# Kernel tuning notes

Hardware: AMD Instinct MI355X
Metric: run time of the kernel (lower is better)

## Reference

```python
import jax, jax.numpy as jnp
import numpy as np

EPS = 1e-8  # torch cosine_similarity denominator clamp


def setup_inputs() -> dict:
    key = jax.random.key(0)
    k1, k2, k3 = jax.random.split(key, 3)
    x = jax.random.normal(k1, (4, 512, 256, 256), dtype=jnp.float32)
    v0 = jax.random.normal(k2, (4, 256, 14, 14), dtype=jnp.float32)
    v1 = jax.random.normal(k3, (4, 256, 14, 14), dtype=jnp.float32)
    return {"x": x, "v0": v0, "v1": v1}


def reference(x, v0, v1):
    # CoLoc_Sel.AV_default_forward with C=2, att_type='cos'
    C = 2
    B, D, F, T = x.shape
    Dc = D // C
    H, W = v0.shape[2], v0.shape[3]

    # AdaptiveMaxPool3d((None,1,1)) on (B,D,F,T): global max over (F,T)
    xp = jnp.max(x, axis=(2, 3)).reshape(B, C, Dc)          # (B,C,Dc) = split blocks
    # x_p1 = blocks in order, x_p2 = reversed; stacked -> permutations P=2
    x_t = jnp.stack([xp, xp[:, ::-1]], axis=1)              # (B,P,C,Dc)

    v_cat = jnp.stack([v0, v1], axis=1)                     # (B,C,Dc,H,W)

    # cosine similarity along the Dc axis, broadcast over P and (H,W)
    dot = jnp.einsum('bpcd,bcdhw->bpchw', x_t, v_cat)       # (B,P,C,H,W)
    xn = jnp.sqrt(jnp.sum(x_t * x_t, axis=3))               # (B,P,C)
    vn = jnp.sqrt(jnp.sum(v_cat * v_cat, axis=2))           # (B,C,H,W)
    maps = dot / jnp.maximum(xn[..., None, None] * vn[:, None], EPS)  # (B,P,C,H,W)

    # per-permutation score: max over (H,W), sum over C
    scores = jnp.sum(jnp.max(maps, axis=(3, 4)), axis=-1)   # (B,P)
    order = jnp.argsort(-scores, axis=1)                    # descending
    ss = jnp.take_along_axis(scores, order, axis=1)
    match_loss = jnp.mean(-ss[:, 0] + jnp.sum(ss[:, 1:], axis=-1))

    maps_sorted = jnp.take_along_axis(maps, order[:, :, None, None, None], axis=1)
    att_maps = maps_sorted[:, 0]                            # (B,C,H,W)

    # pick visual feature vector at argmax spatial location of each att map
    max_ind = jnp.argmax(att_maps.reshape(B, C, H * W), axis=-1)        # (B,C)
    v_flat = v_cat.reshape(B, C, Dc, H * W)
    v_sel = jnp.take_along_axis(v_flat, max_ind[:, :, None, None], axis=3)  # (B,C,Dc,1)

    feats = [jnp.broadcast_to(v_sel[:, c, :, :, None], (B, Dc, F, T)) for c in range(C)]
    out = jnp.concatenate([*feats, x], axis=1)              # (B, 2*D, F, T)
    return out, match_loss, att_maps
```

## Files before the change

### kernel.cpp

```cpp
#include <hip/hip_runtime.h>
#include <hip/hip_bf16.h>
#include <float.h>
#include <math.h>

constexpr int B  = 4;
constexpr int D  = 512;
constexpr int C  = 2;
constexpr int Dc = 256;
constexpr int F  = 256;
constexpr int T  = 256;
constexpr int FT = F * T;
constexpr int H  = 14;
constexpr int W  = 14;
constexpr int HW = H * W;
constexpr int OUTC = 2 * Dc + D;
constexpr float EPSV = 1e-8f;

typedef float f4 __attribute__((ext_vector_type(4)));


__global__ __launch_bounds__(256) void kA_maxcopy(const float* __restrict__ x,
                                                  float* __restrict__ out,
                                                  float* __restrict__ xp) {
    const int slice = blockIdx.x;
    const int b = slice / D;
    const int d = slice % D;
    const f4* xs = (const f4*)(x + (size_t)slice * FT);
    f4* os = (f4*)(out + ((size_t)(b * OUTC + 2 * Dc + d)) * FT);
    float m = -FLT_MAX;
    for (int i0 = threadIdx.x; i0 < FT / 4; i0 += 256 * 8) {
        f4 v[8];
        #pragma unroll
        for (int u = 0; u < 8; ++u)
            v[u] = __builtin_nontemporal_load(&xs[i0 + u * 256]);
        #pragma unroll
        for (int u = 0; u < 8; ++u) {
            __builtin_nontemporal_store(v[u], &os[i0 + u * 256]);
            m = fmaxf(m, fmaxf(fmaxf(v[u].x, v[u].y), fmaxf(v[u].z, v[u].w)));
        }
    }
    for (int off = 32; off; off >>= 1) m = fmaxf(m, __shfl_down(m, off, 64));
    __shared__ float sm[4];
    const int lane = threadIdx.x & 63, wid = threadIdx.x >> 6;
    if (lane == 0) sm[wid] = m;
    __syncthreads();
    if (threadIdx.x == 0) {
        float r = sm[0];
        for (int w2 = 1; w2 < 4; ++w2) r = fmaxf(r, sm[w2]);
        xp[slice] = r;
    }
}

__global__ __launch_bounds__(256) void kB_maps(const float* __restrict__ v0,
                                               const float* __restrict__ v1,
                                               const float* __restrict__ xp,
                                               float* __restrict__ maps,
                                               float* __restrict__ mx,
                                               int* __restrict__ amax) {
    const int bc = blockIdx.x;
    const int b = bc / C, c = bc % C;
    const int tid = threadIdx.x;

    __shared__ float sxc[Dc], sxo[Dc];
    sxc[tid] = xp[(b * C + c) * Dc + tid];
    sxo[tid] = xp[(b * C + (1 - c)) * Dc + tid];
    __syncthreads();

    float ec = sxc[tid] * sxc[tid];
    float eo = sxo[tid] * sxo[tid];
    for (int off = 32; off; off >>= 1) {
        ec += __shfl_down(ec, off, 64);
        eo += __shfl_down(eo, off, 64);
    }
    __shared__ float red[8];
    const int lane = tid & 63, wid = tid >> 6;
    if (lane == 0) { red[wid] = ec; red[4 + wid] = eo; }
    __syncthreads();
    __shared__ float s_xn_c, s_xn_o;
    if (tid == 0) {
        s_xn_c = sqrtf(red[0] + red[1] + red[2] + red[3]);
        s_xn_o = sqrtf(red[4] + red[5] + red[6] + red[7]);
    }
    __syncthreads();
    const float xn_c = s_xn_c, xn_o = s_xn_o;

    float map0 = -FLT_MAX, map1 = -FLT_MAX;
    if (tid < HW) {
        const float* vv = (c == 0 ? v0 : v1) + (size_t)b * Dc * HW;
        float d0 = 0.f, d1 = 0.f, vs = 0.f;
        for (int dc = 0; dc < Dc; ++dc) {
            float v = vv[dc * HW + tid];
            d0 = fmaf(sxc[dc], v, d0);
            d1 = fmaf(sxo[dc], v, d1);
            vs = fmaf(v, v, vs);
        }
        float vn = sqrtf(vs);
        map0 = d0 / fmaxf(xn_c * vn, EPSV);
        map1 = d1 / fmaxf(xn_o * vn, EPSV);
        maps[((b * 2 + 0) * C + c) * HW + tid] = map0;
        maps[((b * 2 + 1) * C + c) * HW + tid] = map1;
    }

    __shared__ float rv[256];
    __shared__ int ri[256];
    for (int p = 0; p < 2; ++p) {
        __syncthreads();
        rv[tid] = (tid < HW) ? (p == 0 ? map0 : map1) : -FLT_MAX;
        ri[tid] = tid;
        __syncthreads();
        for (int s = 128; s; s >>= 1) {
            if (tid < s) {
                float v2 = rv[tid + s]; int i2 = ri[tid + s];
                if (v2 > rv[tid] || (v2 == rv[tid] && i2 < ri[tid])) {
                    rv[tid] = v2; ri[tid] = i2;
                }
            }
            __syncthreads();
        }
        if (tid == 0) {
            mx[(b * 2 + p) * C + c] = rv[0];
            amax[(b * 2 + p) * C + c] = ri[0];
        }
    }
}

__global__ __launch_bounds__(256) void kC_select(const float* __restrict__ maps,
                                                 const float* __restrict__ mx,
                                                 const int* __restrict__ amax,
                                                 float* __restrict__ out,
                                                 int* __restrict__ mind) {
    __shared__ int pbest[B];
    const int tid = threadIdx.x;
    if (tid == 0) {
        float L = 0.f;
        for (int b = 0; b < B; ++b) {
            float s0 = mx[(b * 2 + 0) * C + 0] + mx[(b * 2 + 0) * C + 1];
            float s1 = mx[(b * 2 + 1) * C + 0] + mx[(b * 2 + 1) * C + 1];
            int p = (s1 > s0) ? 1 : 0;
            pbest[b] = p;
            float ss0 = p ? s1 : s0;
            float ss1 = p ? s0 : s1;
            L += (ss1 - ss0);
        }
        out[(size_t)B * OUTC * FT] = L / (float)B;
    }
    __syncthreads();
    const size_t att_off = (size_t)B * OUTC * FT + 1;
    for (int i = tid; i < B * C * HW; i += blockDim.x) {
        int b = i / (C * HW);
        int r = i % (C * HW);
        int c = r / HW;
        int hw = r % HW;
        out[att_off + i] = maps[((b * 2 + pbest[b]) * C + c) * HW + hw];
    }
    if (tid < B * C) {
        int b = tid / C, c = tid % C;
        mind[tid] = amax[(b * 2 + pbest[b]) * C + c];
    }
}

__global__ __launch_bounds__(256) void kD_fill(const float* __restrict__ v0,
                                               const float* __restrict__ v1,
                                               const int* __restrict__ mind,
                                               float* __restrict__ out) {
    const int n = blockIdx.x;
    const int b = n / (2 * Dc);
    const int r = n % (2 * Dc);
    const int c = r / Dc;
    const int dc = r % Dc;
    const int hw = mind[b * C + c];
    const float* vv = (c == 0 ? v0 : v1);
    const float val = vv[((size_t)(b * Dc + dc)) * HW + hw];
    f4 v4 = {val, val, val, val};
    f4* os = (f4*)(out + ((size_t)(b * OUTC + c * Dc + dc)) * FT);
    for (int i0 = threadIdx.x; i0 < FT / 4; i0 += 256 * 8) {
        #pragma unroll
        for (int u = 0; u < 8; ++u)
            __builtin_nontemporal_store(v4, &os[i0 + u * 256]);
    }
}

extern "C" void kernel_launch(void* const* d_in, const int* in_sizes, int n_in,
                              void* d_out, int out_size, void* d_ws, size_t ws_size,
                              hipStream_t stream) {
    const float* x  = (const float*)d_in[0];
    const float* v0 = (const float*)d_in[1];
    const float* v1 = (const float*)d_in[2];
    float* out = (float*)d_out;
    float* ws = (float*)d_ws;

    float* xp   = ws;
    float* maps = ws + 2048;
    float* mx   = ws + 5184;
    int*   amax = (int*)(ws + 5200);
    int*   mind = (int*)(ws + 5216);

    kA_maxcopy<<<B * D, 256, 0, stream>>>(x, out, xp);
    kB_maps<<<B * C, 256, 0, stream>>>(v0, v1, xp, maps, mx, amax);
    kC_select<<<1, 256, 0, stream>>>(maps, mx, amax, out, mind);
    kD_fill<<<B * 2 * Dc, 256, 0, stream>>>(v0, v1, mind, out);
}
```

Baseline: 304.0 us.

## Fuse all stages into one cooperative persistent kernel with grid syncs

```diff
diff --git a/kernel.cpp b/kernel.cpp
--- a/kernel.cpp
+++ b/kernel.cpp
@@ -1,23 +1,180 @@
 #include <hip/hip_runtime.h>
 #include <hip/hip_bf16.h>
+#include <hip/hip_cooperative_groups.h>
 #include <float.h>
 #include <math.h>
+
+namespace cg = cooperative_groups;
 
 constexpr int B  = 4;
 constexpr int D  = 512;
 constexpr int C  = 2;
 constexpr int Dc = 256;
-constexpr int F  = 256;
-constexpr int T  = 256;
-constexpr int FT = F * T;
-constexpr int H  = 14;
-constexpr int W  = 14;
-constexpr int HW = H * W;
+constexpr int FT = 256 * 256;
+constexpr int HW = 14 * 14;
 constexpr int OUTC = 2 * Dc + D;
 constexpr float EPSV = 1e-8f;
 
 typedef float f4 __attribute__((ext_vector_type(4)));
 
+__global__ __launch_bounds__(256, 4) void k_fused(const float* __restrict__ x,
+                                                  const float* __restrict__ v0,
+                                                  const float* __restrict__ v1,
+                                                  float* __restrict__ out,
+                                                  float* __restrict__ ws) {
+    cg::grid_group grid = cg::this_grid();
+    const int tid = threadIdx.x;
+    const int blk = blockIdx.x;
+
+    float* xp   = ws;
+    float* pd0  = ws + 2048;
+    float* pd1  = ws + 10240;
+    float* pvs  = ws + 18432;
+    float* maps = ws + 26624;
+    int*   mind = (int*)(ws + 29760);
+
+    __shared__ float sm[4];
+    __shared__ float s_xn[8];
+    __shared__ float s_mx[16];
+    __shared__ int   s_ai[16];
+    __shared__ int   s_pb[B];
+    __shared__ float cand_v[256];
+    __shared__ int   cand_i[256];
+
+    for (int s = 0; s < 2; ++s) {
+        const int slice = blk * 2 + s;
+        const int b = slice / D, d = slice % D;
+        const f4* xs = (const f4*)(x + (size_t)slice * FT);
+        f4* os = (f4*)(out + ((size_t)(b * OUTC + 2 * Dc + d)) * FT);
+        float m = -FLT_MAX;
+        for (int i0 = tid; i0 < FT / 4; i0 += 256 * 8) {
+            f4 v[8];
+            #pragma unroll
+            for (int u = 0; u < 8; ++u)
+                v[u] = __builtin_nontemporal_load(&xs[i0 + u * 256]);
+            #pragma unroll
+            for (int u = 0; u < 8; ++u) {
+                __builtin_nontemporal_store(v[u], &os[i0 + u * 256]);
+                m = fmaxf(m, fmaxf(fmaxf(v[u].x, v[u].y), fmaxf(v[u].z, v[u].w)));
+            }
+        }
+        for (int off = 32; off; off >>= 1) m = fmaxf(m, __shfl_down(m, off, 64));
+        if ((tid & 63) == 0) sm[tid >> 6] = m;
+        __syncthreads();
+        if (tid == 0) xp[slice] = fmaxf(fmaxf(sm[0], sm[1]), fmaxf(sm[2], sm[3]));
+        __syncthreads();
+    }
+    grid.sync();
+
+    if (blk < 32) {
+        const int b = blk >> 3, c = (blk >> 2) & 1, q = blk & 3;
+        if (tid < HW) {
+            const float* vv = (c == 0 ? v0 : v1) + (size_t)b * Dc * HW;
+            const float* xc = xp + (b * C + c) * Dc;
+            const float* xo = xp + (b * C + (1 - c)) * Dc;
+            float d0 = 0.f, d1 = 0.f, vs = 0.f;
+            for (int dc = q * 64; dc < q * 64 + 64; ++dc) {
+                float v = vv[dc * HW + tid];
+                d0 = fmaf(xc[dc], v, d0);
+                d1 = fmaf(xo[dc], v, d1);
+                vs = fmaf(v, v, vs);
+            }
+            pd0[blk * 256 + tid] = d0;
+            pd1[blk * 256 + tid] = d1;
+            pvs[blk * 256 + tid] = vs;
+        }
+    }
+    grid.sync();
+
+    if (blk == 0) {
+        {
+            const int g = tid >> 5, l = tid & 31;
+            float acc = 0.f;
+            for (int dc = l; dc < Dc; dc += 32) {
+                float v = xp[g * Dc + dc];
+                acc = fmaf(v, v, acc);
+            }
+            for (int off = 16; off; off >>= 1) acc += __shfl_down(acc, off, 32);
+            if (l == 0) s_xn[g] = sqrtf(acc);
+        }
+        __syncthreads();
+        for (int i = tid; i < 16 * HW; i += 256) {
+            const int row = i / HW;
+            const int hw = i % HW;
+            const int b = row >> 2, p = (row >> 1) & 1, c = row & 1;
+            const int base = b * 8 + c * 4;
+            float d = 0.f, vs = 0.f;
+            for (int q = 0; q < 4; ++q) {
+                const int o = (base + q) * 256 + hw;
+                d += (p == 0 ? pd0[o] : pd1[o]);
+                vs += pvs[o];
+            }
+            const float xn = (p == 0) ? s_xn[b * C + c] : s_xn[b * C + (1 - c)];
+            maps[i] = d / fmaxf(xn * sqrtf(vs), EPSV);
+        }
+        __syncthreads();
+        {
+            const int row = tid >> 4, sub = tid & 15;
+            float bv = -FLT_MAX; int bi = HW;
+            for (int hw = sub; hw < HW; hw += 16) {
+                float v = maps[row * HW + hw];
+                if (v > bv) { bv = v; bi = hw; }
+            }
+            cand_v[tid] = bv; cand_i[tid] = bi;
+            __syncthreads();
+            if (sub == 0) {
+                float mv = -FLT_MAX; int mi = 0;
+                for (int k = 0; k < 16; ++k) {
+                    float v = cand_v[row * 16 + k]; int idx = cand_i[row * 16 + k];
+                    if (v > mv || (v == mv && idx < mi)) { mv = v; mi = idx; }
+                }
+                s_mx[row] = mv; s_ai[row] = mi;
+            }
+        }
+        __syncthreads();
+        if (tid == 0) {
+            float L = 0.f;
+            for (int b = 0; b < B; ++b) {
+                const float s0 = s_mx[b * 4 + 0] + s_mx[b * 4 + 1];
+                const float s1 = s_mx[b * 4 + 2] + s_mx[b * 4 + 3];
+                const int p = (s1 > s0) ? 1 : 0;
+                s_pb[b] = p;
+                L += p ? (s0 - s1) : (s1 - s0);
+            }
+            out[(size_t)B * OUTC * FT] = L / (float)B;
+        }
+        __syncthreads();
+        const size_t att_off = (size_t)B * OUTC * FT + 1;
+        for (int i = tid; i < B * C * HW; i += 256) {
+            const int b = i / (C * HW);
+            const int r = i % (C * HW);
+            const int c = r / HW, hw = r % HW;
+            out[att_off + i] = maps[(b * 4 + s_pb[b] * 2 + c) * HW + hw];
+        }
+        if (tid < B * C) {
+            const int b = tid / C, c = tid % C;
+            mind[tid] = s_ai[b * 4 + s_pb[b] * 2 + c];
+        }
+    }
+    grid.sync();
+
+    for (int s = 0; s < 2; ++s) {
+        const int slice = blk * 2 + s;
+        const int b = slice / (2 * Dc);
+        const int r = slice % (2 * Dc);
+        const int c = r / Dc, dc = r % Dc;
+        const int hw = mind[b * C + c];
+        const float* vv = (c == 0 ? v0 : v1);
+        const float val = vv[((size_t)(b * Dc + dc)) * HW + hw];
+        f4 v4 = {val, val, val, val};
+        f4* os = (f4*)(out + ((size_t)(b * OUTC + c * Dc + dc)) * FT);
+        for (int i0 = tid; i0 < FT / 4; i0 += 256 * 8) {
+            #pragma unroll
+            for (int u = 0; u < 8; ++u)
+                __builtin_nontemporal_store(v4, &os[i0 + u * 256]);
+        }
+    }
+}
 
 __global__ __launch_bounds__(256) void kA_maxcopy(const float* __restrict__ x,
                                                   float* __restrict__ out,
@@ -41,13 +198,10 @@
     }
     for (int off = 32; off; off >>= 1) m = fmaxf(m, __shfl_down(m, off, 64));
     __shared__ float sm[4];
-    const int lane = threadIdx.x & 63, wid = threadIdx.x >> 6;
-    if (lane == 0) sm[wid] = m;
+    if ((threadIdx.x & 63) == 0) sm[threadIdx.x >> 6] = m;
     __syncthreads();
     if (threadIdx.x == 0) {
-        float r = sm[0];
-        for (int w2 = 1; w2 < 4; ++w2) r = fmaxf(r, sm[w2]);
-        xp[slice] = r;
+        xp[slice] = fmaxf(fmaxf(sm[0], sm[1]), fmaxf(sm[2], sm[3]));
     }
 }
 
@@ -138,9 +292,7 @@
             float s1 = mx[(b * 2 + 1) * C + 0] + mx[(b * 2 + 1) * C + 1];
             int p = (s1 > s0) ? 1 : 0;
             pbest[b] = p;
-            float ss0 = p ? s1 : s0;
-            float ss1 = p ? s0 : s1;
-            L += (ss1 - ss0);
+            L += p ? (s0 - s1) : (s1 - s0);
         }
         out[(size_t)B * OUTC * FT] = L / (float)B;
     }
@@ -189,14 +341,19 @@
     float* out = (float*)d_out;
     float* ws = (float*)d_ws;
 
-    float* xp   = ws;
-    float* maps = ws + 2048;
-    float* mx   = ws + 5184;
-    int*   amax = (int*)(ws + 5200);
-    int*   mind = (int*)(ws + 5216);
-
-    kA_maxcopy<<<B * D, 256, 0, stream>>>(x, out, xp);
-    kB_maps<<<B * C, 256, 0, stream>>>(v0, v1, xp, maps, mx, amax);
-    kC_select<<<1, 256, 0, stream>>>(maps, mx, amax, out, mind);
-    kD_fill<<<B * 2 * Dc, 256, 0, stream>>>(v0, v1, mind, out);
-}
+    void* args[] = {(void*)&x, (void*)&v0, (void*)&v1, (void*)&out, (void*)&ws};
+    hipError_t err = hipLaunchCooperativeKernel((const void*)k_fused,
+                                                dim3(1024), dim3(256),
+                                                args, 0, stream);
+    if (err != hipSuccess) {
+        float* xp   = ws;
+        float* maps = ws + 2048;
+        float* mx   = ws + 5184;
+        int*   amax = (int*)(ws + 5200);
+        int*   mind = (int*)(ws + 5216);
+        kA_maxcopy<<<B * D, 256, 0, stream>>>(x, out, xp);
+        kB_maps<<<B * C, 256, 0, stream>>>(v0, v1, xp, maps, mx, amax);
+        kC_select<<<1, 256, 0, stream>>>(maps, mx, amax, out, mind);
+        kD_fill<<<B * 2 * Dc, 256, 0, stream>>>(v0, v1, mind, out);
+    }
+}
```

Measured after the change: 658.7 us. +116.6%, slower.
